# Optimization experiments

Measured on AMD Instinct MI355X. Metric: run time of the kernel, lower is better.

The kernel has to match this reference:

```python
import jax, jax.numpy as jnp
import numpy as np

K_AMP = 6.0 ** 0.5      # self.k = sqrt(6) amplification
RES_SCALE = 0.1
EPS_NORM = 5e-05        # F.normalize eps
EPS_KERN = 1e-4         # performer softmax_kernel eps


def setup_inputs() -> dict:
    key = jax.random.key(0)
    ks = jax.random.split(key, 6)
    N, C, H, W = 16, 128, 128, 128
    Cr = C // 2            # reduction=2 -> dim_heads=64
    M = 128                # nb_features
    s = (1.0 / C) ** 0.5   # fan-in scaling for 1x1 conv weights
    return {
        "x": jax.random.normal(ks[0], (N, C, H, W), jnp.float32),
        "w1": jax.random.normal(ks[1], (Cr, C), jnp.float32) * s,
        "b1": jnp.zeros((Cr,), jnp.float32),
        "w2": jax.random.normal(ks[2], (Cr, C), jnp.float32) * s,
        "b2": jnp.zeros((Cr,), jnp.float32),
        "wa": jax.random.normal(ks[3], (C, C), jnp.float32) * s,
        "ba": jnp.zeros((C,), jnp.float32),
        "proj": jax.random.normal(ks[4], (M, Cr), jnp.float32),  # random-feature projection (buffer)
    }


def _l2norm(t):
    n = jnp.linalg.norm(t, axis=-1, keepdims=True)
    return t / jnp.maximum(n, EPS_NORM)


def reference(x, w1, b1, w2, b2, wa, ba, proj):
    N, C, H, W = x.shape
    xt = x.transpose(0, 2, 3, 1).reshape(N, H * W, C)   # [N, HW, C] tokens
    # 1x1 convs == per-token linears
    q = _l2norm(xt @ w1.T + b1) * K_AMP                 # [N, HW, Cr]
    k = _l2norm(xt @ w2.T + b2) * K_AMP                 # [N, HW, Cr]
    v = xt @ wa.T + ba                                  # [N, HW, C]
    # Performer FAVOR+ softmax-kernel feature maps
    d = q.shape[-1]
    dn = d ** -0.25                                     # data normalizer d^(-1/4)
    ratio = proj.shape[0] ** -0.5                       # m^(-1/2)
    qd = jnp.einsum('nid,md->nim', q * dn, proj)        # [N, HW, M]
    kd = jnp.einsum('nid,md->nim', k * dn, proj)
    q_diag = jnp.sum(q * q, axis=-1, keepdims=True) * 0.5 * dn * dn
    k_diag = jnp.sum(k * k, axis=-1, keepdims=True) * 0.5 * dn * dn
    qp = ratio * (jnp.exp(qd - q_diag - jnp.max(qd, axis=-1, keepdims=True)) + EPS_KERN)
    kp = ratio * (jnp.exp(kd - k_diag - jnp.max(kd)) + EPS_KERN)   # global max for keys
    # linear attention: out = (qp @ (kp^T v)) / (qp @ sum(kp))
    ksum = jnp.sum(kp, axis=1)                          # [N, M]
    d_inv = 1.0 / jnp.einsum('nim,nm->ni', qp, ksum)    # [N, HW]
    ctx = jnp.einsum('nim,nie->nme', kp, v)             # [N, M, C]
    out = jnp.einsum('nme,nim,ni->nie', ctx, qp, d_inv) # [N, HW, C]
    return out.transpose(0, 2, 1).reshape(N, C, H, W) * RES_SCALE
```

## Files before the change

### kernel.cpp

```cpp
#include <hip/hip_runtime.h>
#include <hip/hip_bf16.h>
#include <cstdio>
#include <cstdint>

#define HWD 16384
#define NB  16
#define CD  128
#define CR  64
#define MF  128

constexpr float K_AMP = 2.4494897427831781f;
constexpr float DN    = 0.35355339059327379f;
constexpr float RATIO = 0.088388347648318447f;
constexpr float EPSN  = 5e-5f;
constexpr float EPSK  = 1e-4f;
constexpr float RES   = 0.1f;
constexpr float DIAG  = 0.375f;

typedef __attribute__((ext_vector_type(4))) float f32x4;
typedef __attribute__((ext_vector_type(8))) short s16x8;

__device__ __forceinline__ short f2bf(float f) {
  __hip_bfloat16 h = __float2bfloat16(f);
  short s; __builtin_memcpy(&s, &h, 2); return s;
}
__device__ __forceinline__ float bf2f_s(short s) {
  __hip_bfloat16 h; __builtin_memcpy(&h, &s, 2); return __bfloat162float(h);
}
__device__ __forceinline__ f32x4 mfma16(s16x8 a, s16x8 b, f32x4 c) {
  return __builtin_amdgcn_mfma_f32_16x16x32_bf16(a, b, c, 0, 0, 0);
}

constexpr size_t OFF_QP   = 0;
constexpr size_t OFF_EP   = OFF_QP   + 16777216;
constexpr size_t OFF_GP   = OFF_EP   + 16777216;
constexpr size_t OFF_G    = OFF_GP   + 8388608;
constexpr size_t OFF_CTXB = OFF_G    + 262144;
constexpr size_t OFF_KSUM = OFF_CTXB + 131072;
constexpr size_t OFF_XSUM = OFF_KSUM + 2048;
constexpr size_t OFF_KSUMB= OFF_XSUM + 2048;
constexpr size_t OFF_XSUMB= OFF_KSUMB+ 262144;
constexpr size_t OFF_BMAX = OFF_XSUMB+ 262144;
constexpr size_t OFF_SBLK = OFF_BMAX + 2048;
constexpr size_t OFF_W1B  = OFF_SBLK + 2048;
constexpr size_t OFF_W2B  = OFF_W1B  + 4096;
constexpr size_t OFF_PB   = OFF_W2B  + 4096;
constexpr size_t WS_FLOATS = OFF_PB  + 4096;

__global__ void k_prep(const float* __restrict__ w1, const float* __restrict__ w2,
                       const float* __restrict__ proj,
                       short* __restrict__ w1b, short* __restrict__ w2b, short* __restrict__ pb) {
  int t = blockIdx.x * 256 + threadIdx.x;
  w1b[t] = f2bf(w1[t]);
  w2b[t] = f2bf(w2[t]);
  pb[t]  = f2bf(proj[t]);
}

__device__ __forceinline__ void qk_gemms(const short* __restrict__ wb,
                                         const float* __restrict__ bsh,
                                         const short* __restrict__ pb,
                                         const short* Xt, short* Qt,
                                         int tid, f32x4 (&acc2)[8][2]) {
  const int lane = tid & 63, w = tid >> 6;
  const int l15 = lane & 15, q4 = lane >> 4;
  f32x4 acc1[4][2];
  #pragma unroll
  for (int ct = 0; ct < 4; ct++)
    #pragma unroll
    for (int it = 0; it < 2; it++) acc1[ct][it] = {0.f, 0.f, 0.f, 0.f};
  #pragma unroll
  for (int ks = 0; ks < 4; ks++) {
    s16x8 bfr[2];
    #pragma unroll
    for (int it = 0; it < 2; it++)
      bfr[it] = *(const s16x8*)&Xt[(w * 32 + it * 16 + l15) * 136 + ks * 32 + q4 * 8];
    #pragma unroll
    for (int ct = 0; ct < 4; ct++) {
      s16x8 afr = *(const s16x8*)&wb[(ct * 16 + l15) * 128 + ks * 32 + q4 * 8];
      #pragma unroll
      for (int it = 0; it < 2; it++) acc1[ct][it] = mfma16(afr, bfr[it], acc1[ct][it]);
    }
  }
  float qv[4][2][4];
  float ss[2] = {0.f, 0.f};
  #pragma unroll
  for (int ct = 0; ct < 4; ct++)
    #pragma unroll
    for (int it = 0; it < 2; it++)
      #pragma unroll
      for (int r = 0; r < 4; r++) {
        float v = acc1[ct][it][r] + bsh[ct * 16 + q4 * 4 + r];
        qv[ct][it][r] = v;
        ss[it] = fmaf(v, v, ss[it]);
      }
  #pragma unroll
  for (int it = 0; it < 2; it++) {
    ss[it] += __shfl_xor(ss[it], 16);
    ss[it] += __shfl_xor(ss[it], 32);
  }
  float scale[2];
  #pragma unroll
  for (int it = 0; it < 2; it++)
    scale[it] = (K_AMP * DN) / fmaxf(sqrtf(ss[it]), EPSN);
  __syncthreads();
  #pragma unroll
  for (int it = 0; it < 2; it++)
    #pragma unroll
    for (int ct = 0; ct < 4; ct++) {
      short4 pk;
      pk.x = f2bf(qv[ct][it][0] * scale[it]);
      pk.y = f2bf(qv[ct][it][1] * scale[it]);
      pk.z = f2bf(qv[ct][it][2] * scale[it]);
      pk.w = f2bf(qv[ct][it][3] * scale[it]);
      *(short4*)&Qt[(w * 32 + it * 16 + l15) * 72 + ct * 16 + q4 * 4] = pk;
    }
  __syncthreads();
  #pragma unroll
  for (int mt = 0; mt < 8; mt++)
    #pragma unroll
    for (int it = 0; it < 2; it++) acc2[mt][it] = {0.f, 0.f, 0.f, 0.f};
  #pragma unroll
  for (int ks = 0; ks < 2; ks++) {
    s16x8 afr[2];
    #pragma unroll
    for (int it = 0; it < 2; it++)
      afr[it] = *(const s16x8*)&Qt[(w * 32 + it * 16 + l15) * 72 + ks * 32 + q4 * 8];
    #pragma unroll
    for (int mt = 0; mt < 8; mt++) {
      s16x8 bfr = *(const s16x8*)&pb[(mt * 16 + l15) * 64 + ks * 32 + q4 * 8];
      #pragma unroll
      for (int it = 0; it < 2; it++) acc2[mt][it] = mfma16(afr[it], bfr, acc2[mt][it]);
    }
  }
}

__global__ __launch_bounds__(256) void k_qkf(
    const float* __restrict__ x,
    const short* __restrict__ w1b, const float* __restrict__ b1,
    const short* __restrict__ w2b, const float* __restrict__ b2,
    const short* __restrict__ pb,
    short* __restrict__ qp, short* __restrict__ ep,
    float* __restrict__ bmax, float* __restrict__ ksumb, float* __restrict__ xsumb) {
  const int n = blockIdx.y, i0 = blockIdx.x * 128;
  const int tid = threadIdx.x, lane = tid & 63, w = tid >> 6;
  const int l15 = lane & 15, q4 = lane >> 4;
  __shared__ __align__(16) short Xt[128 * 136];
  __shared__ __align__(16) short Qt[128 * 72];
  __shared__ float bsh[128];
  __shared__ float wred[4];
  __shared__ float sred[768];
  if (tid < 64) bsh[tid] = b1[tid];
  else if (tid < 128) bsh[tid] = b2[tid - 64];
  #pragma unroll
  for (int u = 0; u < 16; u++) {
    int id = u * 256 + tid;
    int i = id & 127, cg = id >> 7;
    const float* xp = x + ((size_t)(n * CD + cg * 4) * HWD + i0 + i);
    short4 pk;
    pk.x = f2bf(xp[0]); pk.y = f2bf(xp[HWD]);
    pk.z = f2bf(xp[2 * HWD]); pk.w = f2bf(xp[3 * HWD]);
    *(short4*)&Xt[i * 136 + cg * 4] = pk;
  }
  __syncthreads();

  f32x4 acc2[8][2];

  qk_gemms(w1b, bsh, pb, Xt, Qt, tid, acc2);
  #pragma unroll
  for (int it = 0; it < 2; it++)
    #pragma unroll
    for (int r = 0; r < 4; r++) {
      float mx = -3.0e38f;
      #pragma unroll
      for (int mt = 0; mt < 8; mt++) mx = fmaxf(mx, acc2[mt][it][r]);
      mx = fmaxf(mx, __shfl_xor(mx, 1));
      mx = fmaxf(mx, __shfl_xor(mx, 2));
      mx = fmaxf(mx, __shfl_xor(mx, 4));
      mx = fmaxf(mx, __shfl_xor(mx, 8));
      int i = i0 + w * 32 + it * 16 + q4 * 4 + r;
      #pragma unroll
      for (int mt = 0; mt < 8; mt++) {
        float e = RATIO * (__expf(acc2[mt][it][r] - DIAG - mx) + EPSK);
        qp[((size_t)n * HWD + i) * MF + mt * 16 + l15] = f2bf(e);
      }
    }

  qk_gemms(w2b, bsh + 64, pb, Xt, Qt, tid, acc2);
  float mxk = -3.0e38f;
  #pragma unroll
  for (int mt = 0; mt < 8; mt++)
    #pragma unroll
    for (int it = 0; it < 2; it++)
      #pragma unroll
      for (int r = 0; r < 4; r++) mxk = fmaxf(mxk, acc2[mt][it][r]);
  #pragma unroll
  for (int d = 1; d < 64; d <<= 1) mxk = fmaxf(mxk, __shfl_xor(mxk, d));
  if (lane == 0) wred[w] = mxk;
  __syncthreads();
  const float bm = fmaxf(fmaxf(wred[0], wred[1]), fmaxf(wred[2], wred[3]));
  float es[8];
  #pragma unroll
  for (int mt = 0; mt < 8; mt++) es[mt] = 0.f;
  #pragma unroll
  for (int it = 0; it < 2; it++)
    #pragma unroll
    for (int r = 0; r < 4; r++) {
      int i = i0 + w * 32 + it * 16 + q4 * 4 + r;
      #pragma unroll
      for (int mt = 0; mt < 8; mt++) {
        float e = __expf(acc2[mt][it][r] - bm);
        es[mt] += e;
        ep[((size_t)n * HWD + i) * MF + mt * 16 + l15] = f2bf(e);
      }
    }
  #pragma unroll
  for (int mt = 0; mt < 8; mt++) {
    es[mt] += __shfl_xor(es[mt], 16);
    es[mt] += __shfl_xor(es[mt], 32);
  }
  if (q4 == 0) {
    #pragma unroll
    for (int mt = 0; mt < 8; mt++) sred[w * 128 + mt * 16 + l15] = es[mt];
  }
  {
    int c = tid & 127, half = tid >> 7;
    float xs = 0.f;
    #pragma unroll 16
    for (int u = 0; u < 64; u++) xs += bf2f_s(Xt[(half * 64 + u) * 136 + c]);
    sred[512 + tid] = xs;
  }
  __syncthreads();
  const size_t pb0 = ((size_t)n * 128 + blockIdx.x) * 128;
  if (tid < 128) {
    ksumb[pb0 + tid] = sred[tid] + sred[128 + tid] + sred[256 + tid] + sred[384 + tid];
  } else {
    int c = tid - 128;
    xsumb[pb0 + c] = sred[512 + c] + sred[640 + c];
  }
  if (tid == 0) bmax[n * 128 + blockIdx.x] = bm;
}

__global__ void k_gmax(const float* __restrict__ bmax, float* __restrict__ sblk) {
  __shared__ float red[256];
  int t = threadIdx.x;
  float loc[8], v = -3.0e38f;
  #pragma unroll
  for (int u = 0; u < 8; u++) { loc[u] = bmax[t + 256 * u]; v = fmaxf(v, loc[u]); }
  red[t] = v;
  __syncthreads();
  for (int s = 128; s > 0; s >>= 1) {
    if (t < s) red[t] = fmaxf(red[t], red[t + s]);
    __syncthreads();
  }
  float gm = red[0];
  #pragma unroll
  for (int u = 0; u < 8; u++) sblk[t + 256 * u] = RATIO * __expf(loc[u] - gm - DIAG);
}

__global__ void k_ksum(const float* __restrict__ sblk, const float* __restrict__ ksumb,
                       const float* __restrict__ xsumb, float* __restrict__ ksum,
                       float* __restrict__ xsum) {
  int g = blockIdx.x * 256 + threadIdx.x;
  int n = g >> 7, m = g & 127;
  const float* kb = ksumb + ((size_t)n << 14) + m;
  const float* xb = xsumb + ((size_t)n << 14) + m;
  const float* sb = sblk + n * 128;
  float s = 0.f, xs = 0.f;
  #pragma unroll 4
  for (int b = 0; b < 128; b++) {
    s = fmaf(sb[b], kb[(size_t)b * 128], s);
    xs += xb[(size_t)b * 128];
  }
  ksum[g] = s + RATIO * EPSK * 16384.0f;
  xsum[g] = xs;
}

__global__ __launch_bounds__(256) void k_g(const float* __restrict__ x,
                                           const short* __restrict__ ep,
                                           const float* __restrict__ sblk,
                                           float* __restrict__ gp) {
  const int slab = blockIdx.x, n = blockIdx.y;
  const int t = threadIdx.x, lane = t & 63, w = t >> 6;
  const int l15 = lane & 15, q4 = lane >> 4;
  __shared__ short kl[64 * 136];
  __shared__ short xl[128 * 72];
  f32x4 acc[2][8];
  #pragma unroll
  for (int mt = 0; mt < 2; mt++)
    #pragma unroll
    for (int ct = 0; ct < 8; ct++) acc[mt][ct] = {0.f, 0.f, 0.f, 0.f};
  for (int ch = 0; ch < 8; ch++) {
    int ib = slab * 512 + ch * 64;
    const float sf = sblk[n * 128 + slab * 4 + (ch >> 1)];
    __syncthreads();
    #pragma unroll
    for (int u = 0; u < 4; u++) {
      int id = u * 256 + t, ii = id >> 4, m8 = (id & 15) * 8;
      *(s16x8*)&kl[ii * 136 + m8] =
          *(const s16x8*)&ep[((size_t)n * HWD + ib + ii) * MF + m8];
    }
    #pragma unroll
    for (int u = 0; u < 8; u++) {
      int id = u * 256 + t, c = id >> 4, i4 = (id & 15) * 4;
      const float4 v = *(const float4*)(x + ((size_t)n * CD + c) * HWD + ib + i4);
      short4 pk;
      pk.x = f2bf(v.x * sf); pk.y = f2bf(v.y * sf);
      pk.z = f2bf(v.z * sf); pk.w = f2bf(v.w * sf);
      *(short4*)&xl[c * 72 + i4] = pk;
    }
    __syncthreads();
    #pragma unroll
    for (int ks = 0; ks < 2; ks++) {
      s16x8 afr[2];
      #pragma unroll
      for (int mt = 0; mt < 2; mt++) {
        int m = w * 32 + mt * 16 + l15;
        short tmp[8];
        #pragma unroll
        for (int j = 0; j < 8; j++) tmp[j] = kl[(ks * 32 + q4 * 8 + j) * 136 + m];
        afr[mt] = *(s16x8*)tmp;
      }
      #pragma unroll
      for (int ct = 0; ct < 8; ct++) {
        s16x8 bfr = *(const s16x8*)&xl[(ct * 16 + l15) * 72 + ks * 32 + q4 * 8];
        #pragma unroll
        for (int mt = 0; mt < 2; mt++) acc[mt][ct] = mfma16(afr[mt], bfr, acc[mt][ct]);
      }
    }
  }
  float* g = gp + (((size_t)slab * NB + n) << 14);
  #pragma unroll
  for (int mt = 0; mt < 2; mt++)
    #pragma unroll
    for (int ct = 0; ct < 8; ct++)
      #pragma unroll
      for (int r = 0; r < 4; r++)
        g[(w * 32 + mt * 16 + q4 * 4 + r) * CD + ct * 16 + l15] = acc[mt][ct][r];
}

__global__ void k_gred(const float* __restrict__ gp, const float* __restrict__ xsum,
                       float* __restrict__ G) {
  int t = blockIdx.x * 256 + threadIdx.x;
  int n = t >> 14, r = t & 16383;
  float s = 0.f;
  #pragma unroll
  for (int sc = 0; sc < 32; sc++) s += gp[(((size_t)sc * NB + n) << 14) + r];
  G[((size_t)n << 14) + r] = s + (RATIO * EPSK) * xsum[n * 128 + (r & 127)];
}

__global__ __launch_bounds__(256) void k_ctx(const float* __restrict__ G,
                                             const float* __restrict__ wa,
                                             const float* __restrict__ ba,
                                             const float* __restrict__ ksum,
                                             short* __restrict__ ctxb) {
  int n = blockIdx.x;
  int tm = threadIdx.x & 15, tc = threadIdx.x >> 4;
  const float* Gn = G + ((size_t)n << 14);
  float acc[8][8];
  #pragma unroll
  for (int a = 0; a < 8; a++)
    #pragma unroll
    for (int b = 0; b < 8; b++) acc[a][b] = 0.f;
  for (int c2 = 0; c2 < CD; c2 += 4) {
    float4 g4[8], w4[8];
    #pragma unroll
    for (int a = 0; a < 8; a++) g4[a] = *(const float4*)&Gn[(tm * 8 + a) * CD + c2];
    #pragma unroll
    for (int b = 0; b < 8; b++) w4[b] = *(const float4*)&wa[(tc * 8 + b) * CD + c2];
    #pragma unroll
    for (int a = 0; a < 8; a++)
      #pragma unroll
      for (int b = 0; b < 8; b++) {
        acc[a][b] = fmaf(g4[a].x, w4[b].x, acc[a][b]);
        acc[a][b] = fmaf(g4[a].y, w4[b].y, acc[a][b]);
        acc[a][b] = fmaf(g4[a].z, w4[b].z, acc[a][b]);
        acc[a][b] = fmaf(g4[a].w, w4[b].w, acc[a][b]);
      }
  }
  #pragma unroll
  for (int a = 0; a < 8; a++) {
    int m = tm * 8 + a;
    float km = ksum[n * MF + m];
    #pragma unroll
    for (int b = 0; b < 8; b++) {
      int c = tc * 8 + b;
      ctxb[((size_t)n * CD + c) * MF + m] = f2bf(acc[a][b] + ba[c] * km);
    }
  }
}

__global__ __launch_bounds__(256) void k_out(const short* __restrict__ qp,
                                             const short* __restrict__ ctxb,
                                             const float* __restrict__ ksum,
                                             float* __restrict__ out) {
  const int n = blockIdx.y, i0 = blockIdx.x * 128;
  const int t = threadIdx.x, lane = t & 63, w = t >> 6;
  const int l15 = lane & 15, q4 = lane >> 4;
  __shared__ short qt[128 * 136];
  __shared__ float ksl[128];
  __shared__ float dinv[128];
  if (t < 128) ksl[t] = ksum[n * MF + t];
  #pragma unroll
  for (int u = 0; u < 8; u++) {
    int id = u * 256 + t, i = id >> 4, m8 = (id & 15) * 8;
    *(s16x8*)&qt[i * 136 + m8] =
        *(const s16x8*)&qp[((size_t)n * HWD + i0 + i) * MF + m8];
  }
  __syncthreads();
  if (t < 128) {
    float s = 0.f;
    #pragma unroll
    for (int mb = 0; mb < 16; mb++) {
      s16x8 v = *(const s16x8*)&qt[t * 136 + mb * 8];
      #pragma unroll
      for (int j = 0; j < 8; j++) s = fmaf(bf2f_s(v[j]), ksl[mb * 8 + j], s);
    }
    dinv[t] = RES / s;
  }
  f32x4 acc[8][2];
  #pragma unroll
  for (int it = 0; it < 8; it++)
    #pragma unroll
    for (int ct = 0; ct < 2; ct++) acc[it][ct] = {0.f, 0.f, 0.f, 0.f};
  #pragma unroll
  for (int ks = 0; ks < 4; ks++) {
    s16x8 afr[2];
    #pragma unroll
    for (int ct = 0; ct < 2; ct++)
      afr[ct] = *(const s16x8*)&ctxb[((size_t)n * CD + w * 32 + ct * 16 + l15) * MF +
                                     ks * 32 + q4 * 8];
    #pragma unroll
    for (int it = 0; it < 8; it++) {
      s16x8 bfr = *(const s16x8*)&qt[(it * 16 + l15) * 136 + ks * 32 + q4 * 8];
      #pragma unroll
      for (int ct = 0; ct < 2; ct++) acc[it][ct] = mfma16(afr[ct], bfr, acc[it][ct]);
    }
  }
  __syncthreads();
  #pragma unroll
  for (int it = 0; it < 8; it++) {
    float dv = dinv[it * 16 + l15];
    #pragma unroll
    for (int ct = 0; ct < 2; ct++)
      #pragma unroll
      for (int r = 0; r < 4; r++)
        out[((size_t)n * CD + w * 32 + ct * 16 + q4 * 4 + r) * HWD + i0 + it * 16 + l15] =
            acc[it][ct][r] * dv;
  }
}

extern "C" void kernel_launch(void* const* d_in, const int* in_sizes, int n_in,
                              void* d_out, int out_size, void* d_ws, size_t ws_size,
                              hipStream_t stream) {
  (void)in_sizes; (void)n_in; (void)out_size;
  const float* x    = (const float*)d_in[0];
  const float* w1   = (const float*)d_in[1];
  const float* b1   = (const float*)d_in[2];
  const float* w2   = (const float*)d_in[3];
  const float* b2   = (const float*)d_in[4];
  const float* wa   = (const float*)d_in[5];
  const float* ba   = (const float*)d_in[6];
  const float* proj = (const float*)d_in[7];
  float* ws  = (float*)d_ws;
  float* out = (float*)d_out;

  if (ws_size < WS_FLOATS * sizeof(float)) {
    fprintf(stderr, "ENLCA: workspace too small: need %zu, have %zu\n",
            WS_FLOATS * sizeof(float), ws_size);
  }

  short* qpB   = (short*)(ws + OFF_QP);
  short* epB   = (short*)(ws + OFF_EP);
  float* gpF   = ws + OFF_GP;
  float* GF    = ws + OFF_G;
  short* ctxB  = (short*)(ws + OFF_CTXB);
  float* ksumF = ws + OFF_KSUM;
  float* xsumF = ws + OFF_XSUM;
  float* ksumbF= ws + OFF_KSUMB;
  float* xsumbF= ws + OFF_XSUMB;
  float* bmaxF = ws + OFF_BMAX;
  float* sblkF = ws + OFF_SBLK;
  short* w1B   = (short*)(ws + OFF_W1B);
  short* w2B   = (short*)(ws + OFF_W2B);
  short* pB    = (short*)(ws + OFF_PB);

  k_prep<<<32, 256, 0, stream>>>(w1, w2, proj, w1B, w2B, pB);
  k_qkf<<<dim3(128, 16), 256, 0, stream>>>(x, w1B, b1, w2B, b2, pB,
                                           qpB, epB, bmaxF, ksumbF, xsumbF);
  k_gmax<<<1, 256, 0, stream>>>(bmaxF, sblkF);
  k_ksum<<<8, 256, 0, stream>>>(sblkF, ksumbF, xsumbF, ksumF, xsumF);
  k_g<<<dim3(32, 16), 256, 0, stream>>>(x, epB, sblkF, gpF);
  k_gred<<<1024, 256, 0, stream>>>(gpF, xsumF, GF);
  k_ctx<<<16, 256, 0, stream>>>(GF, wa, ba, ksumF, ctxB);
  k_out<<<dim3(128, 16), 256, 0, stream>>>(qpB, ctxB, ksumF, out);
}
```

Before: 455.9 us.

## Fuse global-max into ksum kernel, alias Qt/sred LDS, drop Qt barriers

Merges the single-block global-max kernel into the ksum kernel: each of the 8 blocks recomputes the global max over bmax, then writes its slice of sblk and keeps the scale factors in LDS for the reduction. This removes one kernel launch and a dependency step. In k_qkf, the Qt and sred shared arrays now share one buffer, which lowers LDS use and may improve occupancy. The two __syncthreads around the Qt writes are removed. That looks safe only if each wave reads just its own Qt rows. It risks a race if sred is written while other waves still read Qt.

```diff
diff --git a/kernel.cpp b/kernel.cpp
--- a/kernel.cpp
+++ b/kernel.cpp
@@ -102,7 +102,6 @@
   #pragma unroll
   for (int it = 0; it < 2; it++)
     scale[it] = (K_AMP * DN) / fmaxf(sqrtf(ss[it]), EPSN);
-  __syncthreads();
   #pragma unroll
   for (int it = 0; it < 2; it++)
     #pragma unroll
@@ -114,7 +113,6 @@
       pk.w = f2bf(qv[ct][it][3] * scale[it]);
       *(short4*)&Qt[(w * 32 + it * 16 + l15) * 72 + ct * 16 + q4 * 4] = pk;
     }
-  __syncthreads();
   #pragma unroll
   for (int mt = 0; mt < 8; mt++)
     #pragma unroll
@@ -145,10 +143,11 @@
   const int tid = threadIdx.x, lane = tid & 63, w = tid >> 6;
   const int l15 = lane & 15, q4 = lane >> 4;
   __shared__ __align__(16) short Xt[128 * 136];
-  __shared__ __align__(16) short Qt[128 * 72];
+  __shared__ __align__(16) char smemQ[128 * 72 * 2];
   __shared__ float bsh[128];
   __shared__ float wred[4];
-  __shared__ float sred[768];
+  short* Qt = (short*)smemQ;
+  float* sred = (float*)smemQ;
   if (tid < 64) bsh[tid] = b1[tid];
   else if (tid < 128) bsh[tid] = b2[tid - 64];
   #pragma unroll
@@ -240,31 +239,31 @@
   if (tid == 0) bmax[n * 128 + blockIdx.x] = bm;
 }
 
-__global__ void k_gmax(const float* __restrict__ bmax, float* __restrict__ sblk) {
+__global__ void k_ksum(const float* __restrict__ bmax, const float* __restrict__ ksumb,
+                       const float* __restrict__ xsumb, float* __restrict__ sblk,
+                       float* __restrict__ ksum, float* __restrict__ xsum) {
   __shared__ float red[256];
+  __shared__ float sb_sh[256];
   int t = threadIdx.x;
-  float loc[8], v = -3.0e38f;
-  #pragma unroll
-  for (int u = 0; u < 8; u++) { loc[u] = bmax[t + 256 * u]; v = fmaxf(v, loc[u]); }
+  float v = -3.0e38f;
+  #pragma unroll
+  for (int u = 0; u < 8; u++) v = fmaxf(v, bmax[t + 256 * u]);
   red[t] = v;
   __syncthreads();
   for (int s = 128; s > 0; s >>= 1) {
     if (t < s) red[t] = fmaxf(red[t], red[t + s]);
     __syncthreads();
   }
-  float gm = red[0];
-  #pragma unroll
-  for (int u = 0; u < 8; u++) sblk[t + 256 * u] = RATIO * __expf(loc[u] - gm - DIAG);
-}
-
-__global__ void k_ksum(const float* __restrict__ sblk, const float* __restrict__ ksumb,
-                       const float* __restrict__ xsumb, float* __restrict__ ksum,
-                       float* __restrict__ xsum) {
-  int g = blockIdx.x * 256 + threadIdx.x;
+  const float gm = red[0];
+  int g = blockIdx.x * 256 + t;
   int n = g >> 7, m = g & 127;
+  float sv = RATIO * __expf(bmax[g] - gm - DIAG);
+  sb_sh[t] = sv;
+  sblk[g] = sv;
+  __syncthreads();
   const float* kb = ksumb + ((size_t)n << 14) + m;
   const float* xb = xsumb + ((size_t)n << 14) + m;
-  const float* sb = sblk + n * 128;
+  const float* sb = &sb_sh[(t >> 7) * 128];
   float s = 0.f, xs = 0.f;
   #pragma unroll 4
   for (int b = 0; b < 128; b++) {
@@ -487,8 +486,7 @@
   k_prep<<<32, 256, 0, stream>>>(w1, w2, proj, w1B, w2B, pB);
   k_qkf<<<dim3(128, 16), 256, 0, stream>>>(x, w1B, b1, w2B, b2, pB,
                                            qpB, epB, bmaxF, ksumbF, xsumbF);
-  k_gmax<<<1, 256, 0, stream>>>(bmaxF, sblkF);
-  k_ksum<<<8, 256, 0, stream>>>(sblkF, ksumbF, xsumbF, ksumF, xsumF);
+  k_ksum<<<8, 256, 0, stream>>>(bmaxF, ksumbF, xsumbF, sblkF, ksumF, xsumF);
   k_g<<<dim3(32, 16), 256, 0, stream>>>(x, epB, sblkF, gpF);
   k_gred<<<1024, 256, 0, stream>>>(gpF, xsumF, GF);
   k_ctx<<<16, 256, 0, stream>>>(GF, wa, ba, ksumF, ctxB);
```

After: 473.9 us. 3.9% more time.
